# Optimization experiments

Measured on AMD Instinct MI355X. Metric: run time of the kernel, lower is better.

The kernel has to match this reference:

```python
import jax, jax.numpy as jnp
import numpy as np

NEG_SLOPE = 0.2  # PyG GATConv default negative_slope


def gat_conv(x, src, dst, W, a_src, a_dst, b, concat):
    """One PyG-style GATConv (with self-loops already in src/dst).
    x: [N, F_in], W: [F_in, H*C], a_src/a_dst: [H, C], b: [H*C] or [C].
    """
    N = x.shape[0]
    H, C = a_src.shape
    h = (x @ W).reshape(N, H, C)                      # [N,H,C]
    al_s = jnp.einsum('nhc,hc->nh', h, a_src)         # [N,H]
    al_d = jnp.einsum('nhc,hc->nh', h, a_dst)
    e = al_s[src] + al_d[dst]                         # [E,H]
    e = jnp.where(e >= 0, e, NEG_SLOPE * e)           # leaky_relu
    # softmax over edges grouped by destination node
    emax = jax.ops.segment_max(e, dst, num_segments=N)  # [N,H]
    ex = jnp.exp(e - emax[dst])
    denom = jax.ops.segment_sum(ex, dst, num_segments=N)
    alpha = ex / denom[dst]                           # [E,H]
    msg = h[src] * alpha[:, :, None]                  # [E,H,C]
    out = jax.ops.segment_sum(msg, dst, num_segments=N)  # [N,H,C]
    out = out.reshape(N, H * C) if concat else out.mean(axis=1)
    return out + b


def setup_inputs() -> dict:
    key = jax.random.key(0)
    ks = jax.random.split(key, 10)
    N, E = 100000, 1600000
    F_in, Hc, H, F_out = 128, 64, 2, 64
    x = jax.random.normal(ks[0], (N, F_in), dtype=jnp.float32)
    edge_index = jax.random.randint(ks[1], (2, E), 0, N, dtype=jnp.int64)
    s1 = 1.0 / np.sqrt(F_in)
    W1 = jax.random.uniform(ks[2], (F_in, H * Hc), jnp.float32, -s1, s1)
    a_src1 = jax.random.normal(ks[3], (H, Hc), jnp.float32) * 0.1
    a_dst1 = jax.random.normal(ks[4], (H, Hc), jnp.float32) * 0.1
    b1 = jnp.zeros((H * Hc,), jnp.float32)
    s2 = 1.0 / np.sqrt(H * Hc)
    W2 = jax.random.uniform(ks[5], (H * Hc, H * F_out), jnp.float32, -s2, s2)
    a_src2 = jax.random.normal(ks[6], (H, F_out), jnp.float32) * 0.1
    a_dst2 = jax.random.normal(ks[7], (H, F_out), jnp.float32) * 0.1
    b2 = jnp.zeros((F_out,), jnp.float32)
    return {"x": x, "edge_index": edge_index,
            "W1": W1, "a_src1": a_src1, "a_dst1": a_dst1, "b1": b1,
            "W2": W2, "a_src2": a_src2, "a_dst2": a_dst2, "b2": b2}


def reference(x, edge_index, W1, a_src1, a_dst1, b1, W2, a_src2, a_dst2, b2):
    N = x.shape[0]
    loops = jnp.arange(N, dtype=edge_index.dtype)
    src = jnp.concatenate([edge_index[0], loops])  # PyG GATConv adds self-loops
    dst = jnp.concatenate([edge_index[1], loops])
    h = gat_conv(x, src, dst, W1, a_src1, a_dst1, b1, concat=True)
    h = jax.nn.elu(h)
    out = gat_conv(h, src, dst, W2, a_src2, a_dst2, b2, concat=False)
    return out
```

## Files before the change

### kernel.cpp

```cpp
#include <hip/hip_runtime.h>
#include <hip/hip_fp16.h>

#define NEG_SLOPE 0.2f
#define LOG2E 1.4426950408889634f

typedef _Float16 half4v __attribute__((ext_vector_type(4)));
typedef _Float16 half8v __attribute__((ext_vector_type(8)));
typedef float f32x4 __attribute__((ext_vector_type(4)));

__device__ inline unsigned enc_max(float f) {
    unsigned b = __float_as_uint(f);
    return (b & 0x80000000u) ? ~b : (b | 0x80000000u);
}
__device__ inline float dec_max(unsigned k) {
    return (k & 0x80000000u) ? __uint_as_float(k ^ 0x80000000u)
                             : __uint_as_float(~k);
}

__global__ __launch_bounds__(256) void gemm_al_kernel(
    const float* __restrict__ X, const float* __restrict__ W,
    const float* __restrict__ asrc, const float* __restrict__ adst,
    __half* __restrict__ H16, float* __restrict__ AL,
    unsigned* __restrict__ ubp, int N)
{
    __shared__ alignas(16) char smem[49152];

    const int t = threadIdx.x, lane = t & 63, wave = t >> 6;
    const int r0 = blockIdx.x * 64;

#pragma unroll
    for (int i = 0; i < 8; i++) {
        const int f = t + i * 256;
        const int row = f >> 5, k4 = f & 31;
        const int k8 = k4 >> 1, hf = k4 & 1;
        float4 v = make_float4(0.f, 0.f, 0.f, 0.f);
        if (r0 + row < N) v = ((const float4*)X)[(size_t)(r0 + row) * 32 + k4];
        half4v h = { (_Float16)v.x, (_Float16)v.y, (_Float16)v.z, (_Float16)v.w };
        const int slot = row * 16 + (k8 ^ (row & 7));
        *(half4v*)(smem + slot * 16 + hf * 8) = h;
    }
    {
        const int c = t >> 1, kh = t & 1;
        const float* Wc = W + c;
#pragma unroll
        for (int i8 = 0; i8 < 8; i8++) {
            const int k0 = kh * 64 + i8 * 8;
            half8v h;
#pragma unroll
            for (int j = 0; j < 8; j++) h[j] = (_Float16)Wc[(size_t)(k0 + j) * 128];
            const int slot = c * 16 + ((k0 >> 3) ^ (c & 7));
            *(half8v*)(smem + 16384 + slot * 16) = h;
        }
    }
    __syncthreads();

    const int mrow = wave * 16 + (lane & 15);
    const int kg = lane >> 4;
    half4v a[8];
#pragma unroll
    for (int ks = 0; ks < 8; ks++) {
        const int k0 = ks * 16 + kg * 4;
        const int slot = mrow * 16 + ((k0 >> 3) ^ (mrow & 7));
        a[ks] = *(const half4v*)(smem + slot * 16 + (k0 & 7) * 2);
    }
    f32x4 acc[8];
#pragma unroll
    for (int ct = 0; ct < 8; ct++) acc[ct] = (f32x4){0.f, 0.f, 0.f, 0.f};
#pragma unroll
    for (int ct = 0; ct < 8; ct++) {
        const int c = ct * 16 + (lane & 15);
        const char* sbase = smem + 16384 + c * 256;
        const int csw = c & 7;
#pragma unroll
        for (int ks = 0; ks < 8; ks++) {
            const int k0 = ks * 16 + kg * 4;
            const int slot = (k0 >> 3) ^ csw;
            half4v b = *(const half4v*)(sbase + slot * 16 + (k0 & 7) * 2);
            acc[ct] = __builtin_amdgcn_mfma_f32_16x16x16f16(a[ks], b, acc[ct], 0, 0, 0);
        }
    }

    float psh0[4] = {0,0,0,0}, psh1[4] = {0,0,0,0};
    float pdh0[4] = {0,0,0,0}, pdh1[4] = {0,0,0,0};
#pragma unroll
    for (int ct = 0; ct < 8; ct++) {
        const int c = ct * 16 + (lane & 15);
        const float as = asrc[c] * LOG2E, ad = adst[c] * LOG2E;
#pragma unroll
        for (int r = 0; r < 4; r++) {
            if (ct < 4) { psh0[r] = fmaf(acc[ct][r], as, psh0[r]);
                          pdh0[r] = fmaf(acc[ct][r], ad, pdh0[r]); }
            else        { psh1[r] = fmaf(acc[ct][r], as, psh1[r]);
                          pdh1[r] = fmaf(acc[ct][r], ad, pdh1[r]); }
        }
    }
#pragma unroll
    for (int off = 1; off <= 8; off <<= 1) {
#pragma unroll
        for (int r = 0; r < 4; r++) {
            psh0[r] += __shfl_xor(psh0[r], off, 64);
            psh1[r] += __shfl_xor(psh1[r], off, 64);
            pdh0[r] += __shfl_xor(pdh0[r], off, 64);
            pdh1[r] += __shfl_xor(pdh1[r], off, 64);
        }
    }
    float rmax0 = -__builtin_inff(), rmax1 = -__builtin_inff();
    if ((lane & 15) == 0) {
#pragma unroll
        for (int r = 0; r < 4; r++) {
            const int gr = r0 + wave * 16 + (lane >> 4) * 4 + r;
            if (gr < N) {
                ((float4*)AL)[gr] = make_float4(psh0[r], psh1[r], pdh0[r], pdh1[r]);
                rmax0 = fmaxf(rmax0, psh0[r]);
                rmax1 = fmaxf(rmax1, psh1[r]);
            }
        }
    }
#pragma unroll
    for (int off = 32; off > 0; off >>= 1) {
        rmax0 = fmaxf(rmax0, __shfl_xor(rmax0, off, 64));
        rmax1 = fmaxf(rmax1, __shfl_xor(rmax1, off, 64));
    }

    __syncthreads();
    float* Dst = (float*)smem;
    float* red = (float*)(smem + 33792);
    if (lane == 0) { red[wave * 2] = rmax0; red[wave * 2 + 1] = rmax1; }
#pragma unroll
    for (int ct = 0; ct < 8; ct++) {
        const int col = ct * 16 + (lane & 15);
        float* drow = Dst + wave * 2112 + ((lane >> 4) * 4) * 132 + col;
#pragma unroll
        for (int r = 0; r < 4; r++) drow[r * 132] = acc[ct][r];
    }
    __syncthreads();
    if (t < 2) {
        float m = fmaxf(fmaxf(red[t], red[2 + t]), fmaxf(red[4 + t], red[6 + t]));
        atomicMax(&ubp[t], enc_max(m));
    }
#pragma unroll
    for (int i = 0; i < 4; i++) {
        const int f = t + i * 256;
        const int row = f >> 4, c16 = f & 15;
        if (r0 + row < N) {
            const float* src = Dst + (row >> 4) * 2112 + (row & 15) * 132 + c16 * 8;
            const float4 v0 = *(const float4*)src;
            const float4 v1 = *(const float4*)(src + 4);
            half8v h = { (_Float16)v0.x, (_Float16)v0.y, (_Float16)v0.z, (_Float16)v0.w,
                         (_Float16)v1.x, (_Float16)v1.y, (_Float16)v1.z, (_Float16)v1.w };
            *(half8v*)((_Float16*)H16 + (size_t)(r0 + row) * 128 + c16 * 8) = h;
        }
    }
}

__global__ void count_kernel(const int* __restrict__ edst, int* __restrict__ cnt,
                             int E, int N, int sliceN, int bps)
{
    const int slice = blockIdx.x & 7;
    const int dlo = slice * sliceN;
    const int dhi = min(N, dlo + sliceN);
    const int Etot = E + N;
    for (int i = (blockIdx.x >> 3) * 256 + (int)threadIdx.x; i < Etot; i += bps * 256) {
        const int d = (i < E) ? edst[i] : (i - E);
        if (d >= dlo && d < dhi) atomicAdd(&cnt[d], 1);
    }
}

__global__ void scan_local_kernel(const int* __restrict__ in, int* __restrict__ out,
                                  int* __restrict__ bsum, int n)
{
    __shared__ int sm[1024];
    const int t = threadIdx.x;
    const int i = blockIdx.x * 1024 + t;
    int v = (i < n) ? in[i] : 0;
    sm[t] = v;
    __syncthreads();
    for (int off = 1; off < 1024; off <<= 1) {
        int x = (t >= off) ? sm[t - off] : 0;
        __syncthreads();
        sm[t] += x;
        __syncthreads();
    }
    if (i < n) out[i] = sm[t];
    if (t == 1023) bsum[blockIdx.x] = sm[t];
}

__global__ void scan_excl_single_kernel(int* __restrict__ a, int B)
{
    __shared__ int sm[1024];
    const int t = threadIdx.x;
    int v = (t < B) ? a[t] : 0;
    sm[t] = v;
    __syncthreads();
    for (int off = 1; off < 1024; off <<= 1) {
        int x = (t >= off) ? sm[t - off] : 0;
        __syncthreads();
        sm[t] += x;
        __syncthreads();
    }
    if (t < B) a[t] = sm[t] - v;
}

__global__ void finalize_csr_kernel(const int* __restrict__ incl,
                                    const int* __restrict__ cnt,
                                    const int* __restrict__ bexcl,
                                    int* __restrict__ dstptr, int* __restrict__ cursor,
                                    int N, int Etot)
{
    const int i = blockIdx.x * 1024 + threadIdx.x;
    if (i < N) {
        int v = incl[i] + bexcl[i >> 10] - cnt[i];
        dstptr[i] = v;
        cursor[i] = v;
    }
    if (i == N) dstptr[N] = Etot;
}

__global__ void scatter_kernel(const int* __restrict__ esrc, const int* __restrict__ edst,
                               int* __restrict__ cursor, int* __restrict__ ssrc,
                               int E, int N, int sliceN, int bps)
{
    const int slice = blockIdx.x & 7;
    const int dlo = slice * sliceN;
    const int dhi = min(N, dlo + sliceN);
    const int Etot = E + N;
    for (int i = (blockIdx.x >> 3) * 256 + (int)threadIdx.x; i < Etot; i += bps * 256) {
        int s, d;
        if (i < E) { s = esrc[i]; d = edst[i]; }
        else       { s = d = i - E; }
        if (d >= dlo && d < dhi) {
            int pos = atomicAdd(&cursor[d], 1);
            ssrc[pos] = s;
        }
    }
}

__global__ __launch_bounds__(256) void aggregate_kernel(
    const __half* __restrict__ H16, const float* __restrict__ AL,
    const int* __restrict__ dstptr, const int* __restrict__ ssrc,
    const unsigned* __restrict__ ubenc, const float* __restrict__ bias,
    float* __restrict__ out, int N, int mode)
{
    const int wid  = (blockIdx.x * blockDim.x + threadIdx.x) >> 6;
    const int lane = threadIdx.x & 63;
    if (wid * 2 >= N) return;
    const int n    = wid * 2 + (lane >> 5);
    const bool act = (n < N);
    const int nn   = act ? n : (N - 1);
    const int beg  = dstptr[nn];
    const int edges = act ? (dstptr[nn + 1] - beg) : 0;
    const int nl   = lane & 31;
    const int head = nl >> 4;

    const float ald = AL[(size_t)nn * 4 + 2 + head];
    float ub = dec_max(ubenc[head]) + ald;
    ub = fmaxf(ub, NEG_SLOPE * ub);

    int tr = (edges + 3) >> 2;
    tr = max(tr, __shfl_xor(tr, 32, 64));
    const int trips = tr;

    float s = 0.f, a0 = 0.f, a1 = 0.f, a2 = 0.f, a3 = 0.f;

    int   sv0[4], sv1[4], sv2[4];
    float e0[4], e1[4], e2[4];
    uint2 g0[4], g1[4], g2[4];

    auto LSRC = [&](int b, int (&sv)[4]) {
#pragma unroll
        for (int k = 0; k < 4; k++) {
            const int idx = 4 * b + k;
            const int v = ssrc[beg + idx];
            sv[k] = (idx < edges) ? v : 0;
        }
    };
    auto LHE = [&](const int (&sv)[4], float (&e)[4], uint2 (&g)[4]) {
#pragma unroll
        for (int k = 0; k < 4; k++) {
            e[k] = AL[(size_t)sv[k] * 4 + head];
            g[k] = ((const uint2*)(H16 + (size_t)sv[k] * 128))[nl];
        }
    };
    auto COMP = [&](int t, const float (&e)[4], const uint2 (&g)[4]) {
        const int rem = edges - 4 * t;
#pragma unroll
        for (int k = 0; k < 4; k++) {
            float tt = e[k] + ald;
            tt = fmaxf(tt, NEG_SLOPE * tt);
            float p = exp2f(tt - ub);
            p = (k < rem) ? p : 0.f;
            s += p;
            const __half2* ph = (const __half2*)&g[k];
            const float2 f01 = __half22float2(ph[0]);
            const float2 f23 = __half22float2(ph[1]);
            a0 = fmaf(p, f01.x, a0);
            a1 = fmaf(p, f01.y, a1);
            a2 = fmaf(p, f23.x, a2);
            a3 = fmaf(p, f23.y, a3);
        }
    };

    LSRC(0, sv0); LSRC(1, sv1); LSRC(2, sv2);
    LHE(sv0, e0, g0);
    LHE(sv1, e1, g1);

    for (int t = 0; t < trips; ) {
        LHE(sv2, e2, g2); LSRC(t + 3, sv0); COMP(t, e0, g0); if (++t == trips) break;
        LHE(sv0, e0, g0); LSRC(t + 3, sv1); COMP(t, e1, g1); if (++t == trips) break;
        LHE(sv1, e1, g1); LSRC(t + 3, sv2); COMP(t, e2, g2); if (++t == trips) break;
    }

    if (!act) return;
    const float inv = 1.f / s;
    float o0 = a0 * inv, o1 = a1 * inv, o2 = a2 * inv, o3 = a3 * inv;

    if (mode == 0) {
        const float4 b4 = ((const float4*)bias)[nl];
        o0 += b4.x; o1 += b4.y; o2 += b4.z; o3 += b4.w;
        o0 = (o0 > 0.f) ? o0 : (__expf(o0) - 1.f);
        o1 = (o1 > 0.f) ? o1 : (__expf(o1) - 1.f);
        o2 = (o2 > 0.f) ? o2 : (__expf(o2) - 1.f);
        o3 = (o3 > 0.f) ? o3 : (__expf(o3) - 1.f);
        ((float4*)out)[(size_t)n * 32 + nl] = make_float4(o0, o1, o2, o3);
    } else {
        const float q0 = __shfl_xor(o0, 16, 64);
        const float q1 = __shfl_xor(o1, 16, 64);
        const float q2 = __shfl_xor(o2, 16, 64);
        const float q3 = __shfl_xor(o3, 16, 64);
        if (nl < 16) {
            const float4 b4 = ((const float4*)bias)[nl];
            ((float4*)out)[(size_t)n * 16 + nl] =
                make_float4(0.5f * (o0 + q0) + b4.x, 0.5f * (o1 + q1) + b4.y,
                            0.5f * (o2 + q2) + b4.z, 0.5f * (o3 + q3) + b4.w);
        }
    }
}

extern "C" void kernel_launch(void* const* d_in, const int* in_sizes, int n_in,
                              void* d_out, int out_size, void* d_ws, size_t ws_size,
                              hipStream_t stream)
{
    const float* x   = (const float*)d_in[0];
    const int*   eix = (const int*)d_in[1];
    const float* W1  = (const float*)d_in[2];
    const float* as1 = (const float*)d_in[3];
    const float* ad1 = (const float*)d_in[4];
    const float* b1  = (const float*)d_in[5];
    const float* W2  = (const float*)d_in[6];
    const float* as2 = (const float*)d_in[7];
    const float* ad2 = (const float*)d_in[8];
    const float* b2  = (const float*)d_in[9];
    float* out = (float*)d_out;

    const int N = in_sizes[0] / 128;
    const int E = in_sizes[1] / 2;
    const int Etot = E + N;
    const int* esrc = eix;
    const int* edst = eix + E;

    char* p = (char*)d_ws;
    __half*   h16    = (__half*)p;   p += (size_t)N * 128 * 2;
    float*    y1     = (float*)p;    p += (size_t)N * 128 * 4;
    float*    al     = (float*)p;    p += (size_t)N * 4 * 4;
    int*      cnt    = (int*)p;      p += (size_t)N * 4;
    unsigned* ub     = (unsigned*)p; p += 64;
    int*      incl   = (int*)p;      p += (size_t)N * 4;
    int*      dstptr = (int*)p;      p += (size_t)(N + 1) * 4;
    int*      cursor = (int*)p;      p += (size_t)N * 4;
    int*      bs1    = (int*)p;      p += 1024 * 4;
    int*      ssrc   = (int*)p;      p += (size_t)(Etot + 256) * 4;

    hipMemsetAsync(cnt, 0, (size_t)N * 4 + 64, stream);
    hipMemsetAsync(ssrc + Etot, 0, 256 * 4, stream);

    {
        const int B0 = (N + 1023) / 1024;
        const int sliceN = (N + 7) / 8;
        const int bps = 512;
        count_kernel<<<bps * 8, 256, 0, stream>>>(edst, cnt, E, N, sliceN, bps);
        scan_local_kernel<<<B0, 1024, 0, stream>>>(cnt, incl, bs1, N);
        scan_excl_single_kernel<<<1, 1024, 0, stream>>>(bs1, B0);
        finalize_csr_kernel<<<(N + 1024) / 1024, 1024, 0, stream>>>(
            incl, cnt, bs1, dstptr, cursor, N, Etot);
        scatter_kernel<<<bps * 8, 256, 0, stream>>>(esrc, edst, cursor, ssrc,
                                                    E, N, sliceN, bps);
    }

    const int ggrid = (N + 63) / 64;
    const int ablocks = (N + 7) / 8;

    gemm_al_kernel<<<ggrid, 256, 0, stream>>>(x, W1, as1, ad1, h16, al, ub, N);
    aggregate_kernel<<<ablocks, 256, 0, stream>>>(h16, al, dstptr, ssrc, ub, b1, y1, N, 0);

    gemm_al_kernel<<<ggrid, 256, 0, stream>>>(y1, W2, as2, ad2, h16, al, ub + 2, N);
    aggregate_kernel<<<ablocks, 256, 0, stream>>>(h16, al, dstptr, ssrc, ub + 2, b2, out, N, 1);
}
```

Baseline: 385.5 us.

## Precompute per-edge softmax weights and pre-transpose weights to fp16 once

Adds a pw_kernel that computes the per-edge exp2 attention weight for both heads once per layer and stores it in an edge-ordered float2 buffer. The aggregate kernel then reads these contiguously instead of doing a random AL gather plus leaky-relu and exp per lane, which was repeated redundantly across the 16 lanes of each head. A separate wprep kernel transposes and converts W1/W2 to fp16 so the GEMM loads weights with coalesced 16-byte reads instead of strided scalar loads. The cost is an extra pass that writes and rereads about 13 MB per layer, and pw_kernel uses one thread per node, which is serial and imbalanced over edges.

```diff
diff --git a/kernel.cpp b/kernel.cpp
--- a/kernel.cpp
+++ b/kernel.cpp
@@ -17,8 +17,19 @@
                              : __uint_as_float(~k);
 }
 
+__global__ void wprep_kernel(const float* __restrict__ W1,
+                             const float* __restrict__ W2,
+                             _Float16* __restrict__ Wt)
+{
+    const int idx = blockIdx.x * 256 + threadIdx.x;
+    const float* W = (idx < 16384) ? W1 : W2;
+    const int i = idx & 16383;
+    const int c = i >> 7, k = i & 127;
+    Wt[idx] = (_Float16)W[k * 128 + c];
+}
+
 __global__ __launch_bounds__(256) void gemm_al_kernel(
-    const float* __restrict__ X, const float* __restrict__ W,
+    const float* __restrict__ X, const _Float16* __restrict__ Wt,
     const float* __restrict__ asrc, const float* __restrict__ adst,
     __half* __restrict__ H16, float* __restrict__ AL,
     unsigned* __restrict__ ubp, int N)
@@ -40,16 +51,13 @@
         *(half4v*)(smem + slot * 16 + hf * 8) = h;
     }
     {
-        const int c = t >> 1, kh = t & 1;
-        const float* Wc = W + c;
-#pragma unroll
-        for (int i8 = 0; i8 < 8; i8++) {
-            const int k0 = kh * 64 + i8 * 8;
-            half8v h;
-#pragma unroll
-            for (int j = 0; j < 8; j++) h[j] = (_Float16)Wc[(size_t)(k0 + j) * 128];
-            const int slot = c * 16 + ((k0 >> 3) ^ (c & 7));
-            *(half8v*)(smem + 16384 + slot * 16) = h;
+        const uint4* Wg = (const uint4*)Wt;
+        uint4* Wl = (uint4*)(smem + 16384);
+#pragma unroll
+        for (int i = 0; i < 8; i++) {
+            const int idx = t + i * 256;
+            const int c = idx >> 4, k8 = idx & 15;
+            Wl[c * 16 + (k8 ^ (c & 7))] = Wg[idx];
         }
     }
     __syncthreads();
@@ -150,6 +158,27 @@
                          (_Float16)v1.x, (_Float16)v1.y, (_Float16)v1.z, (_Float16)v1.w };
             *(half8v*)((_Float16*)H16 + (size_t)(r0 + row) * 128 + c16 * 8) = h;
         }
+    }
+}
+
+__global__ void pw_kernel(const float* __restrict__ AL,
+                          const int* __restrict__ dstptr,
+                          const int* __restrict__ ssrc,
+                          const unsigned* __restrict__ ubenc,
+                          float2* __restrict__ p2, int N)
+{
+    const int n = blockIdx.x * 256 + threadIdx.x;
+    if (n >= N) return;
+    const int beg = dstptr[n], end = dstptr[n + 1];
+    const float ald0 = AL[(size_t)n * 4 + 2];
+    const float ald1 = AL[(size_t)n * 4 + 3];
+    float u0 = dec_max(ubenc[0]) + ald0; u0 = fmaxf(u0, NEG_SLOPE * u0);
+    float u1 = dec_max(ubenc[1]) + ald1; u1 = fmaxf(u1, NEG_SLOPE * u1);
+    for (int e = beg; e < end; e++) {
+        const int s = ssrc[e];
+        float a0 = AL[(size_t)s * 4 + 0] + ald0; a0 = fmaxf(a0, NEG_SLOPE * a0);
+        float a1 = AL[(size_t)s * 4 + 1] + ald1; a1 = fmaxf(a1, NEG_SLOPE * a1);
+        p2[e] = make_float2(exp2f(a0 - u0), exp2f(a1 - u1));
     }
 }
 
@@ -236,10 +265,9 @@
 }
 
 __global__ __launch_bounds__(256) void aggregate_kernel(
-    const __half* __restrict__ H16, const float* __restrict__ AL,
+    const __half* __restrict__ H16, const float* __restrict__ pw,
     const int* __restrict__ dstptr, const int* __restrict__ ssrc,
-    const unsigned* __restrict__ ubenc, const float* __restrict__ bias,
-    float* __restrict__ out, int N, int mode)
+    const float* __restrict__ bias, float* __restrict__ out, int N, int mode)
 {
     const int wid  = (blockIdx.x * blockDim.x + threadIdx.x) >> 6;
     const int lane = threadIdx.x & 63;
@@ -251,10 +279,7 @@
     const int edges = act ? (dstptr[nn + 1] - beg) : 0;
     const int nl   = lane & 31;
     const int head = nl >> 4;
-
-    const float ald = AL[(size_t)nn * 4 + 2 + head];
-    float ub = dec_max(ubenc[head]) + ald;
-    ub = fmaxf(ub, NEG_SLOPE * ub);
+    const float* ph = pw + head;
 
     int tr = (edges + 3) >> 2;
     tr = max(tr, __shfl_xor(tr, 32, 64));
@@ -274,10 +299,10 @@
             sv[k] = (idx < edges) ? v : 0;
         }
     };
-    auto LHE = [&](const int (&sv)[4], float (&e)[4], uint2 (&g)[4]) {
+    auto LHE = [&](int b, const int (&sv)[4], float (&e)[4], uint2 (&g)[4]) {
 #pragma unroll
         for (int k = 0; k < 4; k++) {
-            e[k] = AL[(size_t)sv[k] * 4 + head];
+            e[k] = ph[2 * (beg + 4 * b + k)];
             g[k] = ((const uint2*)(H16 + (size_t)sv[k] * 128))[nl];
         }
     };
@@ -285,14 +310,11 @@
         const int rem = edges - 4 * t;
 #pragma unroll
         for (int k = 0; k < 4; k++) {
-            float tt = e[k] + ald;
-            tt = fmaxf(tt, NEG_SLOPE * tt);
-            float p = exp2f(tt - ub);
-            p = (k < rem) ? p : 0.f;
+            const float p = (k < rem) ? e[k] : 0.f;
             s += p;
-            const __half2* ph = (const __half2*)&g[k];
-            const float2 f01 = __half22float2(ph[0]);
-            const float2 f23 = __half22float2(ph[1]);
+            const __half2* hh = (const __half2*)&g[k];
+            const float2 f01 = __half22float2(hh[0]);
+            const float2 f23 = __half22float2(hh[1]);
             a0 = fmaf(p, f01.x, a0);
             a1 = fmaf(p, f01.y, a1);
             a2 = fmaf(p, f23.x, a2);
@@ -301,13 +323,13 @@
     };
 
     LSRC(0, sv0); LSRC(1, sv1); LSRC(2, sv2);
-    LHE(sv0, e0, g0);
-    LHE(sv1, e1, g1);
+    LHE(0, sv0, e0, g0);
+    LHE(1, sv1, e1, g1);
 
     for (int t = 0; t < trips; ) {
-        LHE(sv2, e2, g2); LSRC(t + 3, sv0); COMP(t, e0, g0); if (++t == trips) break;
-        LHE(sv0, e0, g0); LSRC(t + 3, sv1); COMP(t, e1, g1); if (++t == trips) break;
-        LHE(sv1, e1, g1); LSRC(t + 3, sv2); COMP(t, e2, g2); if (++t == trips) break;
+        LHE(t + 2, sv2, e2, g2); LSRC(t + 3, sv0); COMP(t, e0, g0); if (++t == trips) break;
+        LHE(t + 2, sv0, e0, g0); LSRC(t + 3, sv1); COMP(t, e1, g1); if (++t == trips) break;
+        LHE(t + 2, sv1, e1, g1); LSRC(t + 3, sv2); COMP(t, e2, g2); if (++t == trips) break;
     }
 
     if (!act) return;
@@ -359,20 +381,23 @@
     const int* edst = eix + E;
 
     char* p = (char*)d_ws;
-    __half*   h16    = (__half*)p;   p += (size_t)N * 128 * 2;
-    float*    y1     = (float*)p;    p += (size_t)N * 128 * 4;
-    float*    al     = (float*)p;    p += (size_t)N * 4 * 4;
-    int*      cnt    = (int*)p;      p += (size_t)N * 4;
-    unsigned* ub     = (unsigned*)p; p += 64;
-    int*      incl   = (int*)p;      p += (size_t)N * 4;
-    int*      dstptr = (int*)p;      p += (size_t)(N + 1) * 4;
-    int*      cursor = (int*)p;      p += (size_t)N * 4;
-    int*      bs1    = (int*)p;      p += 1024 * 4;
-    int*      ssrc   = (int*)p;      p += (size_t)(Etot + 256) * 4;
+    __half*    h16    = (__half*)p;    p += (size_t)N * 128 * 2;
+    float*     y1     = (float*)p;     p += (size_t)N * 128 * 4;
+    float*     al     = (float*)p;     p += (size_t)N * 4 * 4;
+    int*       cnt    = (int*)p;       p += (size_t)N * 4;
+    unsigned*  ub     = (unsigned*)p;  p += 64;
+    _Float16*  wt     = (_Float16*)p;  p += 32768 * 2;
+    int*       incl   = (int*)p;       p += (size_t)N * 4;
+    int*       dstptr = (int*)p;       p += (size_t)(N + 1) * 4;
+    int*       cursor = (int*)p;       p += (size_t)N * 4;
+    int*       bs1    = (int*)p;       p += 1024 * 4;
+    float2*    p2     = (float2*)p;    p += (size_t)(Etot + 1024) * 8;
+    int*       ssrc   = (int*)p;       p += (size_t)(Etot + 1024) * 4;
 
     hipMemsetAsync(cnt, 0, (size_t)N * 4 + 64, stream);
-    hipMemsetAsync(ssrc + Etot, 0, 256 * 4, stream);
-
+    hipMemsetAsync(ssrc + Etot, 0, 1024 * 4, stream);
+
+    wprep_kernel<<<128, 256, 0, stream>>>(W1, W2, wt);
     {
         const int B0 = (N + 1023) / 1024;
         const int sliceN = (N + 7) / 8;
@@ -387,11 +412,16 @@
     }
 
     const int ggrid = (N + 63) / 64;
+    const int pblocks = (N + 255) / 256;
     const int ablocks = (N + 7) / 8;
 
-    gemm_al_kernel<<<ggrid, 256, 0, stream>>>(x, W1, as1, ad1, h16, al, ub, N);
-    aggregate_kernel<<<ablocks, 256, 0, stream>>>(h16, al, dstptr, ssrc, ub, b1, y1, N, 0);
-
-    gemm_al_kernel<<<ggrid, 256, 0, stream>>>(y1, W2, as2, ad2, h16, al, ub + 2, N);
-    aggregate_kernel<<<ablocks, 256, 0, stream>>>(h16, al, dstptr, ssrc, ub + 2, b2, out, N, 1);
-}
+    gemm_al_kernel<<<ggrid, 256, 0, stream>>>(x, wt, as1, ad1, h16, al, ub, N);
+    pw_kernel<<<pblocks, 256, 0, stream>>>(al, dstptr, ssrc, ub, p2, N);
+    aggregate_kernel<<<ablocks, 256, 0, stream>>>(h16, (const float*)p2, dstptr,
+                                                  ssrc, b1, y1, N, 0);
+
+    gemm_al_kernel<<<ggrid, 256, 0, stream>>>(y1, wt + 16384, as2, ad2, h16, al, ub + 2, N);
+    pw_kernel<<<pblocks, 256, 0, stream>>>(al, dstptr, ssrc, ub + 2, p2, N);
+    aggregate_kernel<<<ablocks, 256, 0, stream>>>(h16, (const float*)p2, dstptr,
+                                                  ssrc, b2, out, N, 1);
+}
```

After: 423.5 us. +9.9%, slower.
